# Optimization experiments

Measured on AMD Instinct MI355X. Metric: run time of the kernel, lower is better.

The kernel has to match this reference:

```python
import jax, jax.numpy as jnp
import numpy as np

ADAPTER_RATIO = 0.2


def setup_inputs() -> dict:
    key = jax.random.key(0)
    k1, k2, k3, k4, k5 = jax.random.split(key, 5)
    B, D, R, N_DOM, N_TXT = 16384, 1024, 256, 3, 1380
    image_features = jax.random.normal(k1, (B, D), dtype=jnp.float32)
    domain_labels = jax.random.randint(k2, (B,), 0, N_DOM, dtype=jnp.int64)
    W1 = jax.random.normal(k3, (N_DOM, D, R), dtype=jnp.float32) * 0.02
    W2 = jax.random.normal(k4, (N_DOM, R, D), dtype=jnp.float32) * 0.02
    txt = jax.random.normal(k5, (N_TXT, D), dtype=jnp.float32)
    # text features are L2-normalized at module init (encode_text then norm)
    text_features = txt / jnp.linalg.norm(txt, axis=-1, keepdims=True)
    logit_scale = jnp.asarray(np.log(1.0 / 0.07), dtype=jnp.float32)  # CLIP init
    return {
        "image_features": image_features,
        "domain_labels": domain_labels,
        "W1": W1,
        "W2": W2,
        "text_features": text_features,
        "logit_scale": logit_scale,
    }


def reference(image_features, domain_labels, W1, W2, text_features, logit_scale):
    # Domain-routed adapter MLP: run all n_domains experts (n is tiny), then
    # select the routed output per sample (equivalent to the per-sample loop).
    h = jax.nn.relu(jnp.einsum("bd,ndr->bnr", image_features, W1))  # [B,n,R]
    a = jax.nn.relu(jnp.einsum("bnr,nrd->bnd", h, W2))              # [B,n,D]
    idx = domain_labels[:, None, None]                                # [B,1,1]
    adapter_features = jnp.take_along_axis(a, idx, axis=1)[:, 0, :]   # [B,D]
    fused = ADAPTER_RATIO * adapter_features + (1.0 - ADAPTER_RATIO) * image_features
    fused = fused / jnp.linalg.norm(fused, axis=-1, keepdims=True)
    # text_features already normalized; concat over domains done upstream: [N_TXT, D]
    logits = jnp.exp(logit_scale) * (fused @ text_features.T)         # [B, N_TXT]
    return logits
```

## Files before the change

kernel.cpp:

```cpp
#include <hip/hip_runtime.h>
#include <hip/hip_bf16.h>
#include <math.h>

using bf16 = __hip_bfloat16;
typedef __attribute__((ext_vector_type(8))) short bf16x8;
typedef __attribute__((ext_vector_type(4))) float f32x4;
typedef __attribute__((ext_vector_type(4))) unsigned short us4;

#define GAS __attribute__((address_space(1)))
#define LAS __attribute__((address_space(3)))

__device__ __forceinline__ void gload_lds16(const bf16* g, bf16* lds) {
  __builtin_amdgcn_global_load_lds((const GAS void*)g, (LAS void*)lds, 16, 0, 0);
}
__device__ __forceinline__ float b2f(unsigned short u) {
  union { unsigned short s; bf16 b; } x; x.s = u; return __bfloat162float(x.b);
}
__device__ __forceinline__ unsigned short f2b(float f) {
  union { unsigned short s; bf16 b; } x; x.b = __float2bfloat16(f); return x.s;
}

__global__ __launch_bounds__(256) void hist_k(const int* __restrict__ lab,
                                              int* __restrict__ blockHist) {
  const int blk = blockIdx.x, t = threadIdx.x;
  const int lane = t & 63, w = t >> 6;
  const int d = lab[blk * 256 + t];
  __shared__ int wc[4][3];
#pragma unroll
  for (int dd = 0; dd < 3; ++dd) {
    unsigned long long m = __ballot(d == dd);
    if (lane == 0) wc[w][dd] = __popcll(m);
  }
  __syncthreads();
  if (t < 3) blockHist[blk * 3 + t] = wc[0][t] + wc[1][t] + wc[2][t] + wc[3][t];
}

__global__ __launch_bounds__(256) void scan_k(const int* __restrict__ blockHist,
                                              int* __restrict__ blockOff,
                                              int* __restrict__ meta) {
  __shared__ int h[64][3];
  __shared__ int tot[3];
  const int t = threadIdx.x;
  if (t < 192) h[t / 3][t % 3] = blockHist[t];
  __syncthreads();
  if (t < 3) {
    int s = 0;
    for (int b = 0; b < 64; ++b) { int v = h[b][t]; h[b][t] = s; s += v; }
    tot[t] = s;
    meta[t] = s;
  }
  __syncthreads();
  if (t == 0) { meta[4] = 0; meta[5] = tot[0]; meta[6] = tot[0] + tot[1]; }
  if (t < 192) {
    int b = t / 3, d = t % 3;
    int base = (d == 0) ? 0 : (d == 1 ? tot[0] : tot[0] + tot[1]);
    blockOff[t] = base + h[b][d];
  }
}

__global__ __launch_bounds__(256) void scatter2_k(const int* __restrict__ lab,
                                                  const int* __restrict__ blockOff,
                                                  int* __restrict__ perm) {
  const int blk = blockIdx.x, t = threadIdx.x;
  const int lane = t & 63, w = t >> 6;
  const int i = blk * 256 + t;
  const int d = lab[i];
  __shared__ int wc[4][3];
  unsigned long long mymask = 0;
#pragma unroll
  for (int dd = 0; dd < 3; ++dd) {
    unsigned long long m = __ballot(d == dd);
    if (lane == 0) wc[w][dd] = __popcll(m);
    if (dd == d) mymask = m;
  }
  __syncthreads();
  int woff = 0;
  for (int ww = 0; ww < w; ++ww) woff += wc[ww][d];
  const unsigned long long lt = ((unsigned long long)1 << lane) - 1;
  const int rank = blockOff[blk * 3 + d] + woff + __popcll(mymask & lt);
  perm[rank] = i;
}

__global__ __launch_bounds__(256) void cvt_bf16_k(const float* __restrict__ in,
                                                  bf16* __restrict__ out, int n4) {
  int i = blockIdx.x * 256 + threadIdx.x;
  if (i >= n4) return;
  float4 v = ((const float4*)in)[i];
  bf16 t[4] = {__float2bfloat16(v.x), __float2bfloat16(v.y),
               __float2bfloat16(v.z), __float2bfloat16(v.w)};
  ((us4*)out)[i] = *(const us4*)t;
}

__global__ __launch_bounds__(256) void cvt_wt_k(const float* __restrict__ W1,
                                                const float* __restrict__ W2,
                                                const float* __restrict__ txt,
                                                bf16* __restrict__ W1T,
                                                bf16* __restrict__ W2T,
                                                bf16* __restrict__ Tb) {
  int i = blockIdx.x * 256 + threadIdx.x;
  const int n1 = 3 * 256 * 1024;
  const int n2 = n1 + 3 * 1024 * 256;
  const int n3 = n2 + 1536 * 1024;
  if (i < n1) {
    int d = i >> 18, rem = i & 262143;
    int r = rem >> 10, k = rem & 1023;
    W1T[i] = __float2bfloat16(W1[(size_t)d * 262144 + (size_t)k * 256 + r]);
  } else if (i < n2) {
    int j = i - n1;
    int d = j >> 18, rem = j & 262143;
    int n = rem >> 8, k = rem & 255;
    W2T[j] = __float2bfloat16(W2[(size_t)d * 262144 + (size_t)k * 1024 + n]);
  } else if (i < n3) {
    int j = i - n2;
    Tb[j] = (j < 1380 * 1024) ? __float2bfloat16(txt[j]) : __float2bfloat16(0.f);
  }
}

template <bool SEG, bool GATHER_A, bool SCATTER_C, bool RELU, bool C_BF16, bool SCALE>
__global__ __launch_bounds__(256) void gemm_bt(
    const bf16* __restrict__ A, const bf16* __restrict__ BT, void* __restrict__ Cv,
    const int* __restrict__ perm, const int* __restrict__ meta, int Mfull, int N,
    int K, int ldc, int Nvalid, const float* __restrict__ scale_ptr) {
  int cnt = Mfull, base = 0;
  if (SEG) {
    int dom = blockIdx.z;
    cnt = meta[dom];
    base = meta[4 + dom];
    BT += (size_t)dom * N * K;
  }
  const int m0 = blockIdx.x * 128;
  if (m0 >= cnt) return;
  const int n0 = blockIdx.y * 128;

  __shared__ bf16 sA[2][128][32];
  __shared__ bf16 sB[2][128][32];

  const int tid = threadIdx.x;
  const int wid = tid >> 6;
  const int lane = tid & 63;

  const int srow = (wid << 4) + (lane >> 2);
  const int skoff = (lane & 3) << 3;

  int p0 = m0 + srow;       if (p0 > cnt - 1) p0 = cnt - 1;
  int p1 = m0 + srow + 64;  if (p1 > cnt - 1) p1 = cnt - 1;
  long ar0, ar1;
  if (GATHER_A) { ar0 = perm[base + p0]; ar1 = perm[base + p1]; }
  else          { ar0 = base + p0;       ar1 = base + p1; }
  const bf16* a0 = A + (size_t)ar0 * K + skoff;
  const bf16* a1 = A + (size_t)ar1 * K + skoff;
  const bf16* b0 = BT + (size_t)(n0 + srow) * K + skoff;
  const bf16* b1 = BT + (size_t)(n0 + srow + 64) * K + skoff;

  const int fr = lane & 15;
  const int fq = lane >> 4;

  f32x4 acc[4][4];
#pragma unroll
  for (int m = 0; m < 4; ++m)
#pragma unroll
    for (int n = 0; n < 4; ++n) acc[m][n] = (f32x4){0.f, 0.f, 0.f, 0.f};

  const int nk = K >> 5;
  auto stage = [&](int buf, int kt) {
    gload_lds16(a0 + kt * 32, &sA[buf][wid * 16][0]);
    gload_lds16(a1 + kt * 32, &sA[buf][wid * 16 + 64][0]);
    gload_lds16(b0 + kt * 32, &sB[buf][wid * 16][0]);
    gload_lds16(b1 + kt * 32, &sB[buf][wid * 16 + 64][0]);
  };

  stage(0, 0);
  __syncthreads();
  const int wr = wid >> 1, wc = wid & 1;
  for (int kt = 0; kt < nk; ++kt) {
    const int cur = kt & 1;
    if (kt + 1 < nk) stage(cur ^ 1, kt + 1);
    bf16x8 af[4], bfr[4];
#pragma unroll
    for (int m = 0; m < 4; ++m)
      af[m] = *(const bf16x8*)&sA[cur][wr * 64 + m * 16 + fr][fq * 8];
#pragma unroll
    for (int n = 0; n < 4; ++n)
      bfr[n] = *(const bf16x8*)&sB[cur][wc * 64 + n * 16 + fr][fq * 8];
#pragma unroll
    for (int m = 0; m < 4; ++m)
#pragma unroll
      for (int n = 0; n < 4; ++n)
        acc[m][n] = __builtin_amdgcn_mfma_f32_16x16x32_bf16(af[m], bfr[n], acc[m][n], 0, 0, 0);
    __syncthreads();
  }

  float s = 1.f;
  if (SCALE) s = expf(*scale_ptr);
#pragma unroll
  for (int m = 0; m < 4; ++m) {
#pragma unroll
    for (int r = 0; r < 4; ++r) {
      const int p = m0 + wr * 64 + m * 16 + fq * 4 + r;
      if (p < cnt) {
        size_t crow;
        if (SCATTER_C) crow = perm[base + p];
        else if (SEG)  crow = base + p;
        else           crow = p;
#pragma unroll
        for (int n = 0; n < 4; ++n) {
          const int col = n0 + wc * 64 + n * 16 + fr;
          if (col < Nvalid) {
            float v = acc[m][n][r];
            if (RELU) v = fmaxf(v, 0.f);
            v *= s;
            if (C_BF16) ((bf16*)Cv)[crow * (size_t)ldc + col] = __float2bfloat16(v);
            else        ((float*)Cv)[crow * (size_t)ldc + col] = v;
          }
        }
      }
    }
  }
}

__global__ __launch_bounds__(256, 2) void gemm3_occ(
    const bf16* __restrict__ A, const bf16* __restrict__ BT,
    float* __restrict__ C, const float* __restrict__ scale_ptr) {
  extern __shared__ bf16 smem[];
  bf16* sA0 = smem;
  bf16* sB0 = smem + 16384;

  const int tid = threadIdx.x;
  const int lane = tid & 63, wid = tid >> 6;
  const int wr = wid >> 1, wc = wid & 1;
  const int fr = lane & 15, fq = lane >> 4;

  const int bid = blockIdx.x;
  const int x = bid & 7, seq = bid >> 3;
  const int mb = x * 16 + (seq >> 3), nb = seq & 7;
  const int m0 = mb << 7, n0 = nb * 192;

  auto STAGE = [&](int t) {
    const int s = t & 1, koff = t << 6;
    bf16* da = sA0 + (s << 13);
#pragma unroll
    for (int L = 0; L < 4; ++L) {
      const int idx = (L << 8) + tid;
      const int r = idx >> 3, c = idx & 7;
      gload_lds16(A + (size_t)(m0 + r) * 1024 + koff + ((c ^ (r & 7)) << 3),
                  da + ((idx & ~63) << 3));
    }
    bf16* db = sB0 + s * 12288;
#pragma unroll
    for (int L = 0; L < 6; ++L) {
      const int idx = (L << 8) + tid;
      const int r = idx >> 3, c = idx & 7;
      gload_lds16(BT + (size_t)(n0 + r) * 1024 + koff + ((c ^ (r & 7)) << 3),
                  db + ((idx & ~63) << 3));
    }
  };
  auto LDA = [&](int s, int kk, bf16x8* dst) {
    const bf16* base = sA0 + (s << 13);
#pragma unroll
    for (int m = 0; m < 4; ++m) {
      const int row = (wr << 6) + (m << 4) + fr;
      dst[m] = *(const bf16x8*)(base + (row << 6) + ((((kk << 2) + fq) ^ (fr & 7)) << 3));
    }
  };
  auto LDB = [&](int s, int kk, bf16x8* dst) {
    const bf16* base = sB0 + s * 12288;
#pragma unroll
    for (int n = 0; n < 6; ++n) {
      const int row = wc * 96 + (n << 4) + fr;
      dst[n] = *(const bf16x8*)(base + (row << 6) + ((((kk << 2) + fq) ^ (fr & 7)) << 3));
    }
  };

  f32x4 acc[4][6];
#pragma unroll
  for (int m = 0; m < 4; ++m)
#pragma unroll
    for (int n = 0; n < 6; ++n) acc[m][n] = (f32x4){0.f, 0.f, 0.f, 0.f};

  STAGE(0);
  __syncthreads();
  const int nt = 16;
  for (int t = 0; t < nt; ++t) {
    const int s = t & 1;
    if (t + 1 < nt) STAGE(t + 1);
    bf16x8 a0[4], a1[4], b0[6], b1[6];
    LDA(s, 0, a0); LDB(s, 0, b0);
    LDA(s, 1, a1); LDB(s, 1, b1);
#pragma unroll
    for (int m = 0; m < 4; ++m)
#pragma unroll
      for (int n = 0; n < 6; ++n)
        acc[m][n] = __builtin_amdgcn_mfma_f32_16x16x32_bf16(a0[m], b0[n], acc[m][n], 0, 0, 0);
#pragma unroll
    for (int m = 0; m < 4; ++m)
#pragma unroll
      for (int n = 0; n < 6; ++n)
        acc[m][n] = __builtin_amdgcn_mfma_f32_16x16x32_bf16(a1[m], b1[n], acc[m][n], 0, 0, 0);
    __syncthreads();
  }

  const float sc = expf(*scale_ptr);
#pragma unroll
  for (int m = 0; m < 4; ++m) {
    const int grow = m0 + (wr << 6) + (m << 4) + (fq << 2);
#pragma unroll
    for (int r = 0; r < 4; ++r) {
#pragma unroll
      for (int n = 0; n < 6; ++n) {
        const int gcol = n0 + wc * 96 + (n << 4) + fr;
        if (gcol < 1380) C[(size_t)(grow + r) * 1380 + gcol] = acc[m][n][r] * sc;
      }
    }
  }
}

template <bool XB>
__global__ __launch_bounds__(256) void fuse_norm_k(const float* __restrict__ x,
                                                   const bf16* __restrict__ xb,
                                                   bf16* __restrict__ F) {
  const int row = blockIdx.x;
  const int t = threadIdx.x;
  const size_t roff = (size_t)row * 1024;
  us4 av = ((const us4*)(F + roff))[t];
  float xv[4];
  if (XB) {
    us4 xq = ((const us4*)(xb + roff))[t];
#pragma unroll
    for (int j = 0; j < 4; ++j) xv[j] = b2f(xq[j]);
  } else {
    float4 xf = ((const float4*)(x + roff))[t];
    xv[0] = xf.x; xv[1] = xf.y; xv[2] = xf.z; xv[3] = xf.w;
  }
  float f[4];
  float ss = 0.f;
#pragma unroll
  for (int j = 0; j < 4; ++j) {
    f[j] = 0.2f * b2f(av[j]) + 0.8f * xv[j];
    ss += f[j] * f[j];
  }
#pragma unroll
  for (int o = 32; o > 0; o >>= 1) ss += __shfl_down(ss, o);
  __shared__ float sred[4];
  if ((t & 63) == 0) sred[t >> 6] = ss;
  __syncthreads();
  const float rinv = 1.0f / sqrtf(sred[0] + sred[1] + sred[2] + sred[3]);
  us4 ov;
#pragma unroll
  for (int j = 0; j < 4; ++j) ov[j] = f2b(f[j] * rinv);
  ((us4*)(F + roff))[t] = ov;
}

extern "C" void kernel_launch(void* const* d_in, const int* in_sizes, int n_in,
                              void* d_out, int out_size, void* d_ws, size_t ws_size,
                              hipStream_t stream) {
  (void)in_sizes; (void)n_in; (void)out_size;
  const float* x    = (const float*)d_in[0];
  const int*   lab  = (const int*)d_in[1];
  const float* W1   = (const float*)d_in[2];
  const float* W2   = (const float*)d_in[3];
  const float* text = (const float*)d_in[4];
  const float* lsc  = (const float*)d_in[5];
  float* out = (float*)d_out;

  const int B = 16384, D = 1024, R = 256, NTP = 1536;

  char* p = (char*)d_ws;
  auto carve = [&](size_t bytes) {
    char* r = p;
    p += (bytes + 255) & ~(size_t)255;
    return r;
  };
  int*  meta  = (int*)carve(64);
  int*  bhist = (int*)carve(64 * 3 * 4);
  int*  boff  = (int*)carve(64 * 3 * 4);
  int*  perm  = (int*)carve((size_t)B * 4);
  bf16* Xb    = (bf16*)carve((size_t)B * D * 2);
  bf16* W1T   = (bf16*)carve((size_t)3 * R * D * 2);
  bf16* W2T   = (bf16*)carve((size_t)3 * D * R * 2);
  bf16* Tb    = (bf16*)carve((size_t)NTP * D * 2);
  bf16* H     = (bf16*)carve((size_t)B * R * 2);
  bf16* Fb    = (bf16*)carve((size_t)B * D * 2);
  const bool bigws = (size_t)(p - (char*)d_ws) <= ws_size;
  if (!bigws) Fb = Xb;

  hist_k<<<B / 256, 256, 0, stream>>>(lab, bhist);
  scan_k<<<1, 256, 0, stream>>>(bhist, boff, meta);
  scatter2_k<<<B / 256, 256, 0, stream>>>(lab, boff, perm);

  cvt_bf16_k<<<(B * D / 4 + 255) / 256, 256, 0, stream>>>(x, Xb, B * D / 4);
  {
    const int total = 3 * R * D + 3 * D * R + NTP * D;
    cvt_wt_k<<<(total + 255) / 256, 256, 0, stream>>>(W1, W2, text, W1T, W2T, Tb);
  }

  dim3 g1(128, 2, 3);
  gemm_bt<true, true, false, true, true, false><<<g1, 256, 0, stream>>>(
      Xb, W1T, H, perm, meta, B, R, D, R, R, nullptr);
  dim3 g2(128, 8, 3);
  gemm_bt<true, false, true, true, true, false><<<g2, 256, 0, stream>>>(
      H, W2T, Fb, perm, meta, B, D, R, D, D, nullptr);
  if (bigws) fuse_norm_k<true><<<B, 256, 0, stream>>>(x, Xb, Fb);
  else       fuse_norm_k<false><<<B, 256, 0, stream>>>(x, nullptr, Fb);

  gemm3_occ<<<1024, 256, 81920, stream>>>(Fb, Tb, out, lsc);
}
```

Before: 170.2 us.

## Fuse residual mix and norm into GEMM2 epilogue, defer normalization to logits GEMM

The second adapter GEMM's epilogue now computes the 0.2/0.8 residual blend using fp32 x and writes the unnormalized fused row. It also emits per-column-block partial sums of squares. A small rinv kernel reduces these, and the final logits GEMM multiplies by the per-row inverse norm, which removes the separate fuse_norm pass over B×D. In addition, the two conversion kernels are merged into one launch and an XOR swizzle is applied to the LDS chunk layout in gemm_bt to reduce bank conflicts. The trade-off is that the fused rows are rounded to bf16 before normalization rather than after, and the bigws fallback path is dropped.

New measurement: 169.6 us. No clear change (-0.4%).

```diff
diff --git a/kernel.cpp b/kernel.cpp
--- a/kernel.cpp
+++ b/kernel.cpp
@@ -81,46 +81,48 @@
   perm[rank] = i;
 }
 
-__global__ __launch_bounds__(256) void cvt_bf16_k(const float* __restrict__ in,
-                                                  bf16* __restrict__ out, int n4) {
+__global__ __launch_bounds__(256) void cvt_all_k(const float* __restrict__ x,
+                                                 const float* __restrict__ W1,
+                                                 const float* __restrict__ W2,
+                                                 const float* __restrict__ txt,
+                                                 bf16* __restrict__ Xb,
+                                                 bf16* __restrict__ W1T,
+                                                 bf16* __restrict__ W2T,
+                                                 bf16* __restrict__ Tb) {
   int i = blockIdx.x * 256 + threadIdx.x;
-  if (i >= n4) return;
-  float4 v = ((const float4*)in)[i];
-  bf16 t[4] = {__float2bfloat16(v.x), __float2bfloat16(v.y),
-               __float2bfloat16(v.z), __float2bfloat16(v.w)};
-  ((us4*)out)[i] = *(const us4*)t;
-}
-
-__global__ __launch_bounds__(256) void cvt_wt_k(const float* __restrict__ W1,
-                                                const float* __restrict__ W2,
-                                                const float* __restrict__ txt,
-                                                bf16* __restrict__ W1T,
-                                                bf16* __restrict__ W2T,
-                                                bf16* __restrict__ Tb) {
-  int i = blockIdx.x * 256 + threadIdx.x;
+  const int nx = 16384 * 1024 / 4;
+  if (i < nx) {
+    float4 v = ((const float4*)x)[i];
+    bf16 t[4] = {__float2bfloat16(v.x), __float2bfloat16(v.y),
+                 __float2bfloat16(v.z), __float2bfloat16(v.w)};
+    ((us4*)Xb)[i] = *(const us4*)t;
+    return;
+  }
+  int j = i - nx;
   const int n1 = 3 * 256 * 1024;
   const int n2 = n1 + 3 * 1024 * 256;
   const int n3 = n2 + 1536 * 1024;
-  if (i < n1) {
-    int d = i >> 18, rem = i & 262143;
+  if (j < n1) {
+    int d = j >> 18, rem = j & 262143;
     int r = rem >> 10, k = rem & 1023;
-    W1T[i] = __float2bfloat16(W1[(size_t)d * 262144 + (size_t)k * 256 + r]);
-  } else if (i < n2) {
-    int j = i - n1;
-    int d = j >> 18, rem = j & 262143;
+    W1T[j] = __float2bfloat16(W1[(size_t)d * 262144 + (size_t)k * 256 + r]);
+  } else if (j < n2) {
+    int jj = j - n1;
+    int d = jj >> 18, rem = jj & 262143;
     int n = rem >> 8, k = rem & 255;
-    W2T[j] = __float2bfloat16(W2[(size_t)d * 262144 + (size_t)k * 1024 + n]);
-  } else if (i < n3) {
-    int j = i - n2;
-    Tb[j] = (j < 1380 * 1024) ? __float2bfloat16(txt[j]) : __float2bfloat16(0.f);
-  }
-}
-
-template <bool SEG, bool GATHER_A, bool SCATTER_C, bool RELU, bool C_BF16, bool SCALE>
+    W2T[jj] = __float2bfloat16(W2[(size_t)d * 262144 + (size_t)k * 1024 + n]);
+  } else if (j < n3) {
+    int jj = j - n2;
+    Tb[jj] = (jj < 1380 * 1024) ? __float2bfloat16(txt[jj]) : __float2bfloat16(0.f);
+  }
+}
+
+template <bool SEG, bool GATHER_A, int EPI>
 __global__ __launch_bounds__(256) void gemm_bt(
-    const bf16* __restrict__ A, const bf16* __restrict__ BT, void* __restrict__ Cv,
+    const bf16* __restrict__ A, const bf16* __restrict__ BT, bf16* __restrict__ Cv,
     const int* __restrict__ perm, const int* __restrict__ meta, int Mfull, int N,
-    int K, int ldc, int Nvalid, const float* __restrict__ scale_ptr) {
+    int K, int ldc, int Nvalid,
+    const float* __restrict__ xf, float* __restrict__ ssp) {
   int cnt = Mfull, base = 0;
   if (SEG) {
     int dom = blockIdx.z;
@@ -140,7 +142,7 @@
   const int lane = tid & 63;
 
   const int srow = (wid << 4) + (lane >> 2);
-  const int skoff = (lane & 3) << 3;
+  const int skoff = (((lane & 3) ^ ((lane >> 2) & 3)) << 3);
 
   int p0 = m0 + srow;       if (p0 > cnt - 1) p0 = cnt - 1;
   int p1 = m0 + srow + 64;  if (p1 > cnt - 1) p1 = cnt - 1;
@@ -154,6 +156,7 @@
 
   const int fr = lane & 15;
   const int fq = lane >> 4;
+  const int rchunk = (fq ^ (fr & 3)) << 3;
 
   f32x4 acc[4][4];
 #pragma unroll
@@ -178,10 +181,10 @@
     bf16x8 af[4], bfr[4];
 #pragma unroll
     for (int m = 0; m < 4; ++m)
-      af[m] = *(const bf16x8*)&sA[cur][wr * 64 + m * 16 + fr][fq * 8];
+      af[m] = *(const bf16x8*)&sA[cur][wr * 64 + m * 16 + fr][rchunk];
 #pragma unroll
     for (int n = 0; n < 4; ++n)
-      bfr[n] = *(const bf16x8*)&sB[cur][wc * 64 + n * 16 + fr][fq * 8];
+      bfr[n] = *(const bf16x8*)&sB[cur][wc * 64 + n * 16 + fr][rchunk];
 #pragma unroll
     for (int m = 0; m < 4; ++m)
 #pragma unroll
@@ -190,37 +193,73 @@
     __syncthreads();
   }
 
-  float s = 1.f;
-  if (SCALE) s = expf(*scale_ptr);
-#pragma unroll
-  for (int m = 0; m < 4; ++m) {
-#pragma unroll
-    for (int r = 0; r < 4; ++r) {
-      const int p = m0 + wr * 64 + m * 16 + fq * 4 + r;
-      if (p < cnt) {
-        size_t crow;
-        if (SCATTER_C) crow = perm[base + p];
-        else if (SEG)  crow = base + p;
-        else           crow = p;
-#pragma unroll
-        for (int n = 0; n < 4; ++n) {
-          const int col = n0 + wc * 64 + n * 16 + fr;
-          if (col < Nvalid) {
-            float v = acc[m][n][r];
-            if (RELU) v = fmaxf(v, 0.f);
-            v *= s;
-            if (C_BF16) ((bf16*)Cv)[crow * (size_t)ldc + col] = __float2bfloat16(v);
-            else        ((float*)Cv)[crow * (size_t)ldc + col] = v;
+  if (EPI == 0) {
+#pragma unroll
+    for (int m = 0; m < 4; ++m) {
+#pragma unroll
+      for (int r = 0; r < 4; ++r) {
+        const int p = m0 + wr * 64 + m * 16 + fq * 4 + r;
+        if (p < cnt) {
+          const size_t crow = SEG ? (size_t)(base + p) : (size_t)p;
+#pragma unroll
+          for (int n = 0; n < 4; ++n) {
+            const int col = n0 + wc * 64 + n * 16 + fr;
+            if (col < Nvalid)
+              Cv[crow * (size_t)ldc + col] = __float2bfloat16(fmaxf(acc[m][n][r], 0.f));
           }
         }
       }
     }
-  }
+  } else {
+    __shared__ float ssred[128][2];
+#pragma unroll
+    for (int m = 0; m < 4; ++m) {
+#pragma unroll
+      for (int r = 0; r < 4; ++r) {
+        const int lr = wr * 64 + m * 16 + fq * 4 + r;
+        const int p = m0 + lr;
+        float rowss = 0.f;
+        if (p < cnt) {
+          const size_t crow = (size_t)perm[base + p];
+#pragma unroll
+          for (int n = 0; n < 4; ++n) {
+            const int col = n0 + wc * 64 + n * 16 + fr;
+            const float g = 0.2f * fmaxf(acc[m][n][r], 0.f) + 0.8f * xf[crow * 1024 + col];
+            Cv[crow * (size_t)ldc + col] = __float2bfloat16(g);
+            rowss += g * g;
+          }
+        }
+        rowss += __shfl_xor(rowss, 1, 16);
+        rowss += __shfl_xor(rowss, 2, 16);
+        rowss += __shfl_xor(rowss, 4, 16);
+        rowss += __shfl_xor(rowss, 8, 16);
+        if (fr == 0) ssred[lr][wc] = rowss;
+      }
+    }
+    __syncthreads();
+    if (tid < 128) {
+      const int p = m0 + tid;
+      if (p < cnt) {
+        const int crow = perm[base + p];
+        ssp[(size_t)blockIdx.y * 16384 + crow] = ssred[tid][0] + ssred[tid][1];
+      }
+    }
+  }
+}
+
+__global__ __launch_bounds__(256) void rinv_k(const float* __restrict__ ssp,
+                                              float* __restrict__ rinv) {
+  const int r = blockIdx.x * 256 + threadIdx.x;
+  float s = 0.f;
+#pragma unroll
+  for (int b = 0; b < 8; ++b) s += ssp[b * 16384 + r];
+  rinv[r] = rsqrtf(s);
 }
 
 __global__ __launch_bounds__(256, 2) void gemm3_occ(
     const bf16* __restrict__ A, const bf16* __restrict__ BT,
-    float* __restrict__ C, const float* __restrict__ scale_ptr) {
+    float* __restrict__ C, const float* __restrict__ scale_ptr,
+    const float* __restrict__ rinv) {
   extern __shared__ bf16 smem[];
   bf16* sA0 = smem;
   bf16* sB0 = smem + 16384;
@@ -305,55 +344,20 @@
     const int grow = m0 + (wr << 6) + (m << 4) + (fq << 2);
 #pragma unroll
     for (int r = 0; r < 4; ++r) {
+      const float rv = sc * rinv[grow + r];
 #pragma unroll
       for (int n = 0; n < 6; ++n) {
         const int gcol = n0 + wc * 96 + (n << 4) + fr;
-        if (gcol < 1380) C[(size_t)(grow + r) * 1380 + gcol] = acc[m][n][r] * sc;
+        if (gcol < 1380) C[(size_t)(grow + r) * 1380 + gcol] = acc[m][n][r] * rv;
       }
     }
   }
-}
-
-template <bool XB>
-__global__ __launch_bounds__(256) void fuse_norm_k(const float* __restrict__ x,
-                                                   const bf16* __restrict__ xb,
-                                                   bf16* __restrict__ F) {
-  const int row = blockIdx.x;
-  const int t = threadIdx.x;
-  const size_t roff = (size_t)row * 1024;
-  us4 av = ((const us4*)(F + roff))[t];
-  float xv[4];
-  if (XB) {
-    us4 xq = ((const us4*)(xb + roff))[t];
-#pragma unroll
-    for (int j = 0; j < 4; ++j) xv[j] = b2f(xq[j]);
-  } else {
-    float4 xf = ((const float4*)(x + roff))[t];
-    xv[0] = xf.x; xv[1] = xf.y; xv[2] = xf.z; xv[3] = xf.w;
-  }
-  float f[4];
-  float ss = 0.f;
-#pragma unroll
-  for (int j = 0; j < 4; ++j) {
-    f[j] = 0.2f * b2f(av[j]) + 0.8f * xv[j];
-    ss += f[j] * f[j];
-  }
-#pragma unroll
-  for (int o = 32; o > 0; o >>= 1) ss += __shfl_down(ss, o);
-  __shared__ float sred[4];
-  if ((t & 63) == 0) sred[t >> 6] = ss;
-  __syncthreads();
-  const float rinv = 1.0f / sqrtf(sred[0] + sred[1] + sred[2] + sred[3]);
-  us4 ov;
-#pragma unroll
-  for (int j = 0; j < 4; ++j) ov[j] = f2b(f[j] * rinv);
-  ((us4*)(F + roff))[t] = ov;
 }
 
 extern "C" void kernel_launch(void* const* d_in, const int* in_sizes, int n_in,
                               void* d_out, int out_size, void* d_ws, size_t ws_size,
                               hipStream_t stream) {
-  (void)in_sizes; (void)n_in; (void)out_size;
+  (void)in_sizes; (void)n_in; (void)out_size; (void)ws_size;
   const float* x    = (const float*)d_in[0];
   const int*   lab  = (const int*)d_in[1];
   const float* W1   = (const float*)d_in[2];
@@ -370,37 +374,35 @@
     p += (bytes + 255) & ~(size_t)255;
     return r;
   };
-  int*  meta  = (int*)carve(64);
-  int*  bhist = (int*)carve(64 * 3 * 4);
-  int*  boff  = (int*)carve(64 * 3 * 4);
-  int*  perm  = (int*)carve((size_t)B * 4);
-  bf16* Xb    = (bf16*)carve((size_t)B * D * 2);
-  bf16* W1T   = (bf16*)carve((size_t)3 * R * D * 2);
-  bf16* W2T   = (bf16*)carve((size_t)3 * D * R * 2);
-  bf16* Tb    = (bf16*)carve((size_t)NTP * D * 2);
-  bf16* H     = (bf16*)carve((size_t)B * R * 2);
-  bf16* Fb    = (bf16*)carve((size_t)B * D * 2);
-  const bool bigws = (size_t)(p - (char*)d_ws) <= ws_size;
-  if (!bigws) Fb = Xb;
+  int*   meta  = (int*)carve(64);
+  int*   bhist = (int*)carve(64 * 3 * 4);
+  int*   boff  = (int*)carve(64 * 3 * 4);
+  int*   perm  = (int*)carve((size_t)B * 4);
+  float* ssp   = (float*)carve((size_t)8 * B * 4);
+  float* rinv  = (float*)carve((size_t)B * 4);
+  bf16*  Xb    = (bf16*)carve((size_t)B * D * 2);
+  bf16*  W1T   = (bf16*)carve((size_t)3 * R * D * 2);
+  bf16*  W2T   = (bf16*)carve((size_t)3 * D * R * 2);
+  bf16*  Tb    = (bf16*)carve((size_t)NTP * D * 2);
+  bf16*  H     = (bf16*)carve((size_t)B * R * 2);
+  bf16*  Fb    = (bf16*)carve((size_t)B * D * 2);
 
   hist_k<<<B / 256, 256, 0, stream>>>(lab, bhist);
   scan_k<<<1, 256, 0, stream>>>(bhist, boff, meta);
   scatter2_k<<<B / 256, 256, 0, stream>>>(lab, boff, perm);
 
-  cvt_bf16_k<<<(B * D / 4 + 255) / 256, 256, 0, stream>>>(x, Xb, B * D / 4);
   {
-    const int total = 3 * R * D + 3 * D * R + NTP * D;
-    cvt_wt_k<<<(total + 255) / 256, 256, 0, stream>>>(W1, W2, text, W1T, W2T, Tb);
+    const int nx = B * D / 4;
+    const int total = nx + 3 * R * D + 3 * D * R + NTP * D;
+    cvt_all_k<<<(total + 255) / 256, 256, 0, stream>>>(x, W1, W2, text, Xb, W1T, W2T, Tb);
   }
 
   dim3 g1(128, 2, 3);
-  gemm_bt<true, true, false, true, true, false><<<g1, 256, 0, stream>>>(
-      Xb, W1T, H, perm, meta, B, R, D, R, R, nullptr);
+  gemm_bt<true, true, 0><<<g1, 256, 0, stream>>>(
+      Xb, W1T, H, perm, meta, B, R, D, R, R, nullptr, nullptr);
   dim3 g2(128, 8, 3);
-  gemm_bt<true, false, true, true, true, false><<<g2, 256, 0, stream>>>(
-      H, W2T, Fb, perm, meta, B, D, R, D, D, nullptr);
-  if (bigws) fuse_norm_k<true><<<B, 256, 0, stream>>>(x, Xb, Fb);
-  else       fuse_norm_k<false><<<B, 256, 0, stream>>>(x, nullptr, Fb);
-
-  gemm3_occ<<<1024, 256, 81920, stream>>>(Fb, Tb, out, lsc);
-}
+  gemm_bt<true, false, 1><<<g2, 256, 0, stream>>>(
+      H, W2T, Fb, perm, meta, B, D, R, D, D, x, ssp);
+  rinv_k<<<B / 256, 256, 0, stream>>>(ssp, rinv);
+  gemm3_occ<<<1024, 256, 81920, stream>>>(Fb, Tb, out, lsc, rinv);
+}
```
